# Optimization experiments

Measured on AMD Instinct MI355X. Metric: run time of the kernel, lower is better.

The kernel has to match this reference:

```python
import jax, jax.numpy as jnp
import numpy as np

L, H, HD, D, FF, V, S_LEN = 12, 12, 64, 768, 3072, 50257, 1024
NEG = jnp.finfo(jnp.float32).min


def _ln(x, g, b, eps=1e-5):
    mu = x.mean(-1, keepdims=True)
    var = ((x - mu) ** 2).mean(-1, keepdims=True)
    return (x - mu) * jax.lax.rsqrt(var + eps) * g + b


def setup_inputs() -> dict:
    key = jax.random.key(0)
    ks = jax.random.split(key, 14)
    n = lambda k, shp, s=0.02: jax.random.normal(k, shp, jnp.float32) * s
    return {
        "input_ids": jax.random.randint(ks[0], (1, S_LEN), 0, V, dtype=jnp.int32),
        "attention_mask": jnp.ones((1, S_LEN), jnp.int32),
        "wte": n(ks[1], (V, D)),
        "wpe": n(ks[2], (S_LEN, D)),
        "ln1_g": 1.0 + n(ks[3], (L, D), 0.01),
        "ln1_b": n(ks[4], (L, D), 0.01),
        "W_qkv": n(ks[5], (L, D, 3 * D)),
        "b_qkv": n(ks[6], (L, 3 * D)),
        "W_o": n(ks[7], (L, D, D)),
        "b_o": n(ks[8], (L, D)),
        "ln2_g": 1.0 + n(ks[9], (L, D), 0.01),
        "ln2_b": n(ks[10], (L, D), 0.01),
        "W_fc": n(ks[11], (L, D, FF)),
        "b_fc": n(ks[12], (L, FF)),
        "W_proj": n(ks[13], (L, FF, D)),
        "b_proj": jnp.zeros((L, D), jnp.float32),
        "S": 20, "Sa1": 21, "S2": 600,
    }


def reference(input_ids, attention_mask, wte, wpe, ln1_g, ln1_b, W_qkv, b_qkv,
              W_o, b_o, ln2_g, ln2_b, W_fc, b_fc, W_proj, b_proj, S, Sa1, S2):
    T = input_ids.shape[-1]
    h0 = wte[input_ids[0]] + wpe[:T]                      # [T, D]
    causal = jnp.tril(jnp.ones((T, T), bool))
    add_mask = (1.0 - attention_mask[0].astype(jnp.float32)) * NEG  # [T]
    scale = 1.0 / np.sqrt(HD).astype(np.float32)

    def step(h, p):
        (l1g, l1b, Wqkv, bqkv, Wo, bo, l2g, l2b, Wfc, bfc, Wp, bp) = p
        xl = _ln(h, l1g, l1b)                             # pre-block LN, [T, D]
        # ---- standard GPT-2 block forward (advances hidden state) ----
        qkv = xl @ Wqkv + bqkv
        q, k, v = jnp.split(qkv, 3, axis=-1)
        q = q.reshape(T, H, HD).transpose(1, 0, 2)        # [H, T, HD]
        k = k.reshape(T, H, HD).transpose(1, 0, 2)
        v = v.reshape(T, H, HD).transpose(1, 0, 2)
        sc = jnp.einsum('hqd,hkd->hqk', q, k) * scale
        sc = jnp.where(causal, sc, NEG) + add_mask
        ctx = jnp.einsum('hqk,hkd->hqd', jax.nn.softmax(sc, axis=-1), v)
        attn_out = ctx.transpose(1, 0, 2).reshape(T, D) @ Wo + bo
        h2 = h + attn_out
        h_new = h2 + (jax.nn.gelu(_ln(h2, l2g, l2b) @ Wfc + bfc,
                                  approximate=True) @ Wp + bp)
        # ---- manual QK circuit decomposition (pre-block hidden state) ----
        Wq, Wk, _ = jnp.split(Wqkv, 3, axis=1)            # [D, D] each
        bq, bk, _ = jnp.split(bqkv, 3, axis=0)            # [D] each
        Wmhq = Wq.reshape(D, H, HD).transpose(1, 0, 2)    # [H, D, HD]
        Wmhk = Wk.reshape(D, H, HD).transpose(1, 0, 2)
        bqh = bq.reshape(H, HD)                           # [H, HD]
        bkh = bk.reshape(H, HD)
        qc = jnp.einsum('td,hdk->htk', xl, Wmhq)          # x W_q per head
        kc = jnp.einsum('td,hdk->htk', xl, Wmhk)          # x W_k per head
        term1 = jnp.einsum('hqk,htk->hqt', qc, kc)                 # x Wq Wk^T x^T
        term2 = jnp.einsum('hk,htk->ht', bqh, kc)[:, None, :]      # bq Wk^T x^T
        term3 = jnp.einsum('hqk,hk->hq', qc, bkh)[:, :, None]      # x Wq bk^T
        term4 = jnp.einsum('hk,hk->h', bqh, bkh)[:, None, None]    # bq bk^T
        scores = (term1 + term2 + term3 + term4) * scale
        aw = jax.nn.softmax(jnp.where(causal, scores, NEG), axis=-1)  # [H, T, T]
        dup = aw[:, S2, S]
        ind = aw[:, S2, Sa1]
        prev = aw[:, -1, S2]
        return h_new, (dup, ind, prev, prev)

    params = (ln1_g, ln1_b, W_qkv, b_qkv, W_o, b_o,
              ln2_g, ln2_b, W_fc, b_fc, W_proj, b_proj)
    _, (dup, ind, prev, name) = jax.lax.scan(step, h0, params)
    return dup, ind, prev, name   # each [L, H] = [12, 12]
```

## Files before the change

### kernel.cpp

```cpp
#include <hip/hip_runtime.h>
#include <hip/hip_bf16.h>
#include <math.h>

namespace {

constexpr int T = 1024;
constexpr int D = 768;
constexpr int FF = 3072;
constexpr int H = 12;
constexpr int HD = 64;
constexpr int L = 12;
constexpr float SCALE = 0.125f;
constexpr float MNEG = -1.0e30f;

typedef __attribute__((ext_vector_type(8))) short short8;
typedef __attribute__((ext_vector_type(4))) float floatx4;

__device__ inline unsigned short f2bf(float f) {
    __hip_bfloat16 h = __float2bfloat16(f);
    return *reinterpret_cast<unsigned short*>(&h);
}
__device__ inline float bf2f(unsigned short u) {
    union { unsigned int i; float f; } c;
    c.i = (unsigned int)u << 16;
    return c.f;
}
__device__ inline void gld16(const void* g, void* l) {
    __builtin_amdgcn_global_load_lds(
        (const __attribute__((address_space(1))) void*)g,
        (__attribute__((address_space(3))) void*)l, 16, 0, 0);
}

__global__ void embed_kernel(const int* __restrict__ ids,
                             const float* __restrict__ wte,
                             const float* __restrict__ wpe,
                             float* __restrict__ h) {
    int i = blockIdx.x * blockDim.x + threadIdx.x;
    if (i >= T * D) return;
    int t = i / D, d = i % D;
    h[i] = wte[(long)ids[t] * D + d] + wpe[i];
}

__global__ __launch_bounds__(256)
void ln_kernel(const float* __restrict__ x, const float* __restrict__ g,
               const float* __restrict__ b, unsigned short* __restrict__ out) {
    int row = blockIdx.x, tid = threadIdx.x;
    const float* xr = x + (long)row * D;
    float v0 = xr[tid], v1 = xr[tid + 256], v2 = xr[tid + 512];
    __shared__ float red[4];
    __shared__ float share;
    float s = v0 + v1 + v2;
#pragma unroll
    for (int o = 32; o; o >>= 1) s += __shfl_down(s, o, 64);
    if ((tid & 63) == 0) red[tid >> 6] = s;
    __syncthreads();
    if (tid == 0) share = (red[0] + red[1] + red[2] + red[3]) * (1.0f / D);
    __syncthreads();
    float mu = share;
    float d0 = v0 - mu, d1 = v1 - mu, d2 = v2 - mu;
    float q = d0 * d0 + d1 * d1 + d2 * d2;
#pragma unroll
    for (int o = 32; o; o >>= 1) q += __shfl_down(q, o, 64);
    __syncthreads();
    if ((tid & 63) == 0) red[tid >> 6] = q;
    __syncthreads();
    if (tid == 0) share = rsqrtf((red[0] + red[1] + red[2] + red[3]) * (1.0f / D) + 1e-5f);
    __syncthreads();
    float rs = share;
    unsigned short* orow = out + (long)row * D;
    orow[tid]       = f2bf(d0 * rs * g[tid]       + b[tid]);
    orow[tid + 256] = f2bf(d1 * rs * g[tid + 256] + b[tid + 256]);
    orow[tid + 512] = f2bf(d2 * rs * g[tid + 512] + b[tid + 512]);
}

__global__ __launch_bounds__(256)
void wconvert_b(const float* __restrict__ W, unsigned short* __restrict__ WT,
                int K, int N) {
    const int zl = blockIdx.z;
    W  += (long)zl * K * N;
    WT += (long)zl * N * K;
    __shared__ float t[32][33];
    const int n0 = blockIdx.x * 32, k0 = blockIdx.y * 32;
    const int tx = threadIdx.x, ty = threadIdx.y;
#pragma unroll
    for (int i = 0; i < 4; i++)
        t[ty * 4 + i][tx] = W[(long)(k0 + ty * 4 + i) * N + n0 + tx];
    __syncthreads();
#pragma unroll
    for (int i = 0; i < 4; i++)
        WT[(long)(n0 + ty * 4 + i) * K + k0 + tx] = f2bf(t[tx][ty * 4 + i]);
}

#define GEMM_CORE(KLEN)                                                                 \
    floatx4 acc[2][4] = {};                                                             \
    gld16(ApA, &As[0][ablk][0][0]);                                                     \
    gld16(ApB, &As[0][ablk + 4][0][0]);                                                 \
    gld16(Bp,  &Bs[0][ablk][0][0]);                                                     \
    __syncthreads();                                                                    \
    const int nsteps = (KLEN) >> 5;                                                     \
    for (int s = 0; s < nsteps; s++) {                                                  \
        const int buf = s & 1;                                                          \
        const int nb = buf ^ 1;                                                         \
        if (s + 1 < nsteps) {                                                           \
            gld16(ApA + (s + 1) * 32, &As[nb][ablk][0][0]);                             \
            gld16(ApB + (s + 1) * 32, &As[nb][ablk + 4][0][0]);                         \
            gld16(Bp  + (s + 1) * 32, &Bs[nb][ablk][0][0]);                             \
        }                                                                               \
        short8 af[2], bfr[4];                                                           \
        _Pragma("unroll")                                                               \
        for (int mi = 0; mi < 2; mi++)                                                  \
            af[mi] = *(const short8*)&As[buf][w * 2 + mi][lane][0];                     \
        _Pragma("unroll")                                                               \
        for (int ni = 0; ni < 4; ni++)                                                  \
            bfr[ni] = *(const short8*)&Bs[buf][ni][lane][0];                            \
        _Pragma("unroll")                                                               \
        for (int mi = 0; mi < 2; mi++)                                                  \
            _Pragma("unroll")                                                           \
            for (int ni = 0; ni < 4; ni++)                                              \
                acc[mi][ni] = __builtin_amdgcn_mfma_f32_16x16x32_bf16(                  \
                    af[mi], bfr[ni], acc[mi][ni], 0, 0, 0);                             \
        __syncthreads();                                                                \
    }

#define GEMM_PRELUDE(KOFF)                                                              \
    const int tid = threadIdx.x;                                                        \
    const int w = tid >> 6, lane = tid & 63;                                            \
    const int ablk = tid >> 6;                                                          \
    const int sl = tid & 63;                                                            \
    const int row0 = blockIdx.y * 128, col0 = blockIdx.x * 64;                          \
    __shared__ unsigned short As[2][8][64][8];                                          \
    __shared__ unsigned short Bs[2][4][64][8];                                          \
    const unsigned short* ApA = A + (long)(row0 + ablk * 16 + (sl & 15)) * K + (KOFF) + (sl >> 4) * 8; \
    const unsigned short* ApB = ApA + 64L * K;                                          \
    const unsigned short* Bp  = BT + (long)(col0 + ablk * 16 + (sl & 15)) * K + (KOFF) + (sl >> 4) * 8;

__global__ __launch_bounds__(256)
void gemm_fused(const unsigned short* __restrict__ A, const unsigned short* __restrict__ BT,
                const float* __restrict__ bias, unsigned short* __restrict__ Cb,
                int N, int K, int flags) {
    GEMM_PRELUDE(0)
    GEMM_CORE(K)
#pragma unroll
    for (int mi = 0; mi < 2; mi++) {
        int rg = row0 + (w * 2 + mi) * 16 + (lane >> 4) * 4;
#pragma unroll
        for (int ni = 0; ni < 4; ni++) {
            int cg = col0 + ni * 16 + (lane & 15);
            float bv = (flags & 1) ? bias[cg] : 0.f;
            float bscale = ((flags & 16) && cg < D) ? SCALE : 1.0f;
#pragma unroll
            for (int r = 0; r < 4; r++) {
                float v = acc[mi][ni][r] + bv;
                if (flags & 4) {
                    float zz = 0.7978845608028654f * (v + 0.044715f * v * v * v);
                    v = v / (1.0f + __expf(-2.0f * zz));
                }
                Cb[(long)(rg + r) * N + cg] = f2bf(v * bscale);
            }
        }
    }
}

__global__ __launch_bounds__(256)
void gemm_bf16(const unsigned short* __restrict__ A, const unsigned short* __restrict__ BT,
               float* __restrict__ part, int N, int K, int splitK) {
    const int z = blockIdx.z;
    const int Kc = K / splitK;
    GEMM_PRELUDE(z * Kc)
    GEMM_CORE(Kc)
    float* dst = part + (long)z * T * N;
#pragma unroll
    for (int mi = 0; mi < 2; mi++) {
        int rg = row0 + (w * 2 + mi) * 16 + (lane >> 4) * 4;
#pragma unroll
        for (int ni = 0; ni < 4; ni++) {
            int cg = col0 + ni * 16 + (lane & 15);
#pragma unroll
            for (int r = 0; r < 4; r++)
                dst[(long)(rg + r) * N + cg] = acc[mi][ni][r];
        }
    }
}

__global__ __launch_bounds__(256)
void reduce_ln(const float* __restrict__ part, const float* __restrict__ bias,
               const float* __restrict__ resid,
               const float* __restrict__ g, const float* __restrict__ b,
               float* __restrict__ Cres, unsigned short* __restrict__ Cln,
               int splitK) {
    const int row = blockIdx.x, tid = threadIdx.x;
    const int c0 = tid, c1 = tid + 256, c2 = tid + 512;
    const long rb = (long)row * D;
    float v0 = bias[c0] + resid[rb + c0];
    float v1 = bias[c1] + resid[rb + c1];
    float v2 = bias[c2] + resid[rb + c2];
    for (int z = 0; z < splitK; z++) {
        const float* p = part + (long)z * T * D + rb;
        v0 += p[c0]; v1 += p[c1]; v2 += p[c2];
    }
    float* crow = Cres + rb;
    crow[c0] = v0; crow[c1] = v1; crow[c2] = v2;
    __shared__ float red[4];
    __shared__ float share;
    float s = v0 + v1 + v2;
#pragma unroll
    for (int o = 32; o; o >>= 1) s += __shfl_down(s, o, 64);
    if ((tid & 63) == 0) red[tid >> 6] = s;
    __syncthreads();
    if (tid == 0) share = (red[0] + red[1] + red[2] + red[3]) * (1.0f / D);
    __syncthreads();
    float mu = share;
    float d0 = v0 - mu, d1 = v1 - mu, d2 = v2 - mu;
    float q = d0 * d0 + d1 * d1 + d2 * d2;
#pragma unroll
    for (int o = 32; o; o >>= 1) q += __shfl_down(q, o, 64);
    __syncthreads();
    if ((tid & 63) == 0) red[tid >> 6] = q;
    __syncthreads();
    if (tid == 0) share = rsqrtf((red[0] + red[1] + red[2] + red[3]) * (1.0f / D) + 1e-5f);
    __syncthreads();
    float rs = share;
    unsigned short* orow = Cln + rb;
    orow[c0] = f2bf(d0 * rs * g[c0] + b[c0]);
    orow[c1] = f2bf(d1 * rs * g[c1] + b[c1]);
    orow[c2] = f2bf(d2 * rs * g[c2] + b[c2]);
}

__device__ void probe_body(const unsigned short* __restrict__ qkvb,
                           const int* __restrict__ Sp, const int* __restrict__ Sa1p,
                           const int* __restrict__ S2p,
                           float* __restrict__ out, int layer, int which, int h) {
    const int s = *Sp, sa1 = *Sa1p, s2 = *S2p;
    const int row = which ? (T - 1) : s2;
    const int tid = threadIdx.x;
    __shared__ float qrow[64];
    __shared__ float prob[T];
    __shared__ float red[4];
    __shared__ float bshare;
    if (tid < 64) qrow[tid] = bf2f(qkvb[(long)row * (3 * D) + h * HD + tid]);
    __syncthreads();
    float mloc = -INFINITY;
    for (int j = tid; j <= row; j += 256) {
        const unsigned short* krow = qkvb + (long)j * (3 * D) + D + h * HD;
        float acc = 0;
#pragma unroll
        for (int d = 0; d < 64; d += 8) {
            short8 kv = *(const short8*)(krow + d);
#pragma unroll
            for (int e = 0; e < 8; e++)
                acc += qrow[d + e] * bf2f((unsigned short)kv[e]);
        }
        prob[j] = acc;
        mloc = fmaxf(mloc, acc);
    }
#pragma unroll
    for (int o = 32; o; o >>= 1) mloc = fmaxf(mloc, __shfl_down(mloc, o, 64));
    if ((tid & 63) == 0) red[tid >> 6] = mloc;
    __syncthreads();
    if (tid == 0) bshare = fmaxf(fmaxf(red[0], red[1]), fmaxf(red[2], red[3]));
    __syncthreads();
    float m = bshare;
    float ssum = 0;
    for (int j = tid; j <= row; j += 256) {
        float e = expf(prob[j] - m);
        prob[j] = e;
        ssum += e;
    }
#pragma unroll
    for (int o = 32; o; o >>= 1) ssum += __shfl_down(ssum, o, 64);
    __syncthreads();
    if ((tid & 63) == 0) red[tid >> 6] = ssum;
    __syncthreads();
    if (tid == 0) bshare = red[0] + red[1] + red[2] + red[3];
    __syncthreads();
    float inv = 1.0f / bshare;
    if (tid == 0) {
        if (which == 0) {
            out[0 * (L * H) + layer * H + h] = prob[s] * inv;
            out[1 * (L * H) + layer * H + h] = prob[sa1] * inv;
        } else {
            out[2 * (L * H) + layer * H + h] = prob[s2] * inv;
            out[3 * (L * H) + layer * H + h] = prob[s2] * inv;
        }
    }
}

__global__ __launch_bounds__(256)
void probe_kernel(const unsigned short* __restrict__ qkvb,
                  const int* __restrict__ Sp, const int* __restrict__ Sa1p,
                  const int* __restrict__ S2p,
                  float* __restrict__ out, int layer) {
    probe_body(qkvb, Sp, Sa1p, S2p, out, layer, blockIdx.x, blockIdx.y);
}

__global__ __launch_bounds__(256)
void flash_probe(const unsigned short* __restrict__ qkvb, unsigned short* __restrict__ ctxb,
                 const int* __restrict__ Sp, const int* __restrict__ Sa1p,
                 const int* __restrict__ S2p, float* __restrict__ out, int layer) {
    const int h = blockIdx.y;
    if (blockIdx.x >= T / 32) {
        probe_body(qkvb, Sp, Sa1p, S2p, out, layer, blockIdx.x - T / 32, h);
        return;
    }
    const int q0 = blockIdx.x * 32;
    const int tid = threadIdx.x;
    const int w = tid >> 6;
    const int pair = w >> 1;
    const int sub = w & 1;
    const int l = tid & 63;
    const int lm = l & 15;
    const int g = l >> 4;

    __shared__ unsigned short Kl[64][72];
    __shared__ unsigned short Vt[64][80];
    __shared__ unsigned short Pl[4][16][72];

    const int qw = q0 + pair * 16;

    short8 qf[2];
    {
        const unsigned short* qp = qkvb + (long)(qw + lm) * (3 * D) + h * HD + g * 8;
        qf[0] = *(const short8*)(qp);
        qf[1] = *(const short8*)(qp + 32);
    }

    const int d8 = (tid & 7) * 8;
    const int kp = (tid >> 3) * 2;

    float m = MNEG, lsum = 0.f;
    floatx4 o[4] = {};
    const int nt = blockIdx.x / 2 + 1;

    for (int t = 0; t < nt; t++) {
        const int c0 = t * 64;
        __syncthreads();
        {
            const unsigned short* kr0 = qkvb + (long)(c0 + kp) * (3 * D) + D + h * HD + d8;
            const unsigned short* kr1 = kr0 + 3 * D;
            *(short8*)&Kl[kp][d8]     = *(const short8*)kr0;
            *(short8*)&Kl[kp + 1][d8] = *(const short8*)kr1;
            short8 va = *(const short8*)(kr0 + D);
            short8 vb = *(const short8*)(kr1 + D);
#pragma unroll
            for (int j = 0; j < 8; j++) {
                unsigned int pk = (unsigned)(unsigned short)va[j] |
                                  ((unsigned)(unsigned short)vb[j] << 16);
                *(unsigned int*)&Vt[d8 + j][kp] = pk;
            }
        }
        __syncthreads();

        floatx4 st[2] = {};
#pragma unroll
        for (int ks = 0; ks < 2; ks++)
#pragma unroll
            for (int m2 = 0; m2 < 2; m2++) {
                short8 af = *(const short8*)&Kl[(sub * 2 + m2) * 16 + lm][ks * 32 + g * 8];
                st[m2] = __builtin_amdgcn_mfma_f32_16x16x32_bf16(af, qf[ks], st[m2], 0, 0, 0);
            }

        const int qg = qw + lm;
        const int cb = c0 + sub * 32;
        if (cb + 31 > qw) {
#pragma unroll
            for (int m2 = 0; m2 < 2; m2++)
#pragma unroll
                for (int r = 0; r < 4; r++)
                    if (cb + m2 * 16 + g * 4 + r > qg) st[m2][r] = MNEG;
        }
        float tmax = fmaxf(fmaxf(fmaxf(st[0][0], st[0][1]), fmaxf(st[0][2], st[0][3])),
                           fmaxf(fmaxf(st[1][0], st[1][1]), fmaxf(st[1][2], st[1][3])));
        tmax = fmaxf(tmax, __shfl_xor(tmax, 16));
        tmax = fmaxf(tmax, __shfl_xor(tmax, 32));
        float mn = fmaxf(m, tmax);
        float alpha = __expf(m - mn);
        float psum = 0.f;
        unsigned short pb[8];
#pragma unroll
        for (int m2 = 0; m2 < 2; m2++)
#pragma unroll
            for (int r = 0; r < 4; r++) {
                float p = __expf(st[m2][r] - mn);
                psum += p;
                pb[m2 * 4 + r] = f2bf(p);
            }
        lsum = lsum * alpha + psum;
        m = mn;
#pragma unroll
        for (int m2 = 0; m2 < 2; m2++) {
            unsigned int p0 = (unsigned)pb[m2 * 4 + 0] | ((unsigned)pb[m2 * 4 + 1] << 16);
            unsigned int p1 = (unsigned)pb[m2 * 4 + 2] | ((unsigned)pb[m2 * 4 + 3] << 16);
            *(unsigned int*)&Pl[w][lm][(sub * 2 + m2) * 16 + g * 4]     = p0;
            *(unsigned int*)&Pl[w][lm][(sub * 2 + m2) * 16 + g * 4 + 2] = p1;
        }
        float ar0 = __shfl(alpha, g * 4 + 0), ar1 = __shfl(alpha, g * 4 + 1);
        float ar2 = __shfl(alpha, g * 4 + 2), ar3 = __shfl(alpha, g * 4 + 3);
#pragma unroll
        for (int fd = 0; fd < 4; fd++) {
            o[fd][0] *= ar0; o[fd][1] *= ar1; o[fd][2] *= ar2; o[fd][3] *= ar3;
        }
        {
            short8 pa = *(const short8*)&Pl[w][lm][sub * 32 + g * 8];
#pragma unroll
            for (int fd = 0; fd < 4; fd++) {
                short8 vb = *(const short8*)&Vt[fd * 16 + lm][sub * 32 + g * 8];
                o[fd] = __builtin_amdgcn_mfma_f32_16x16x32_bf16(pa, vb, o[fd], 0, 0, 0);
            }
        }
    }
    float l2 = lsum + __shfl_xor(lsum, 16);
    float l4 = l2 + __shfl_xor(l2, 32);

    float* Om = (float*)&Kl[0][0];
    float2* Mlb = (float2*)((char*)Om + 2 * 16 * 68 * 4);
    __syncthreads();
    if (sub == 1) {
        if (g == 0) Mlb[pair * 16 + lm] = make_float2(m, l4);
#pragma unroll
        for (int fd = 0; fd < 4; fd++)
#pragma unroll
            for (int r = 0; r < 4; r++)
                Om[(pair * 16 + g * 4 + r) * 68 + fd * 16 + lm] = o[fd][r];
    }
    __syncthreads();
    if (sub == 0) {
        float2 oth = Mlb[pair * 16 + lm];
        float M = fmaxf(m, oth.x);
        float e0 = __expf(m - M), e1 = __expf(oth.x - M);
        float inv = 1.0f / (l4 * e0 + oth.y * e1);
        float a0 = e0 * inv, a1 = e1 * inv;
#pragma unroll
        for (int fd = 0; fd < 4; fd++) {
            unsigned short* cp = ctxb + (long)(qw + g * 4) * D + h * HD + fd * 16 + lm;
#pragma unroll
            for (int r = 0; r < 4; r++) {
                float w0r = __shfl(a0, g * 4 + r);
                float w1r = __shfl(a1, g * 4 + r);
                float val = o[fd][r] * w0r +
                            Om[(pair * 16 + g * 4 + r) * 68 + fd * 16 + lm] * w1r;
                cp[(long)r * D] = f2bf(val);
            }
        }
    }
}

}

extern "C" void kernel_launch(void* const* d_in, const int* in_sizes, int n_in,
                              void* d_out, int out_size, void* d_ws, size_t ws_size,
                              hipStream_t stream) {
    const int*   ids    = (const int*)  d_in[0];
    const float* wte    = (const float*)d_in[2];
    const float* wpe    = (const float*)d_in[3];
    const float* ln1_g  = (const float*)d_in[4];
    const float* ln1_b  = (const float*)d_in[5];
    const float* W_qkv  = (const float*)d_in[6];
    const float* b_qkv  = (const float*)d_in[7];
    const float* W_o    = (const float*)d_in[8];
    const float* b_o    = (const float*)d_in[9];
    const float* ln2_g  = (const float*)d_in[10];
    const float* ln2_b  = (const float*)d_in[11];
    const float* W_fc   = (const float*)d_in[12];
    const float* b_fc   = (const float*)d_in[13];
    const float* W_proj = (const float*)d_in[14];
    const float* b_proj = (const float*)d_in[15];
    const int*   Sp     = (const int*)  d_in[16];
    const int*   Sa1p   = (const int*)  d_in[17];
    const int*   S2p    = (const int*)  d_in[18];
    float* out = (float*)d_out;

    float* ws   = (float*)d_ws;
    float* h    = ws;
    float* h2   = h   + (long)T * D;
    float* part = h2  + (long)T * D;
    unsigned short* xl   = (unsigned short*)(part + 4L * T * D);
    unsigned short* qkvb = xl   + (long)T * D;
    unsigned short* ctxb = qkvb + (long)T * 3 * D;
    unsigned short* fb   = ctxb + (long)T * D;
    unsigned short* wt_qkv  = fb      + (long)T * FF;
    unsigned short* wt_o    = wt_qkv  + (long)L * 3 * D * D;
    unsigned short* wt_fc   = wt_o    + (long)L * D * D;
    unsigned short* wt_proj = wt_fc   + (long)L * D * FF;

    embed_kernel<<<(T * D + 255) / 256, 256, 0, stream>>>(ids, wte, wpe, h);
    wconvert_b<<<dim3(3 * D / 32, D / 32, L), dim3(32, 8), 0, stream>>>(W_qkv, wt_qkv, D, 3 * D);
    wconvert_b<<<dim3(D / 32, D / 32, L), dim3(32, 8), 0, stream>>>(W_o, wt_o, D, D);
    wconvert_b<<<dim3(FF / 32, D / 32, L), dim3(32, 8), 0, stream>>>(W_fc, wt_fc, D, FF);
    wconvert_b<<<dim3(D / 32, FF / 32, L), dim3(32, 8), 0, stream>>>(W_proj, wt_proj, FF, D);
    ln_kernel<<<T, 256, 0, stream>>>(h, ln1_g, ln1_b, xl);

    for (int l = 0; l < L; l++) {
        gemm_fused<<<dim3(3 * D / 64, T / 128), 256, 0, stream>>>(
            xl, wt_qkv + (long)l * 3 * D * D, b_qkv + (long)l * 3 * D,
            qkvb, 3 * D, D, 1 | 16);

        if (l == L - 1) {
            probe_kernel<<<dim3(2, H), 256, 0, stream>>>(qkvb, Sp, Sa1p, S2p, out, l);
            break;
        }

        flash_probe<<<dim3(T / 32 + 2, H), 256, 0, stream>>>(
            qkvb, ctxb, Sp, Sa1p, S2p, out, l);
        gemm_bf16<<<dim3(D / 64, T / 128, 4), 256, 0, stream>>>(
            ctxb, wt_o + (long)l * D * D, part, D, D, 4);
        reduce_ln<<<T, 256, 0, stream>>>(
            part, b_o + (long)l * D, h, ln2_g + l * D, ln2_b + l * D, h2, xl, 4);
        gemm_fused<<<dim3(FF / 64, T / 128), 256, 0, stream>>>(
            xl, wt_fc + (long)l * D * FF, b_fc + (long)l * FF, fb, FF, D, 1 | 4);
        gemm_bf16<<<dim3(D / 64, T / 128, 4), 256, 0, stream>>>(
            fb, wt_proj + (long)l * D * FF, part, D, FF, 4);
        reduce_ln<<<T, 256, 0, stream>>>(
            part, b_proj + (long)l * D, h2, ln1_g + (l + 1) * D, ln1_b + (l + 1) * D, h, xl, 4);
    }
}
```

Before: 1.338 ms.

## Double GEMM K-step to 64 and load attention K fragments directly from global

The shared GEMM core now stages 64-wide K slices per pipeline step (two 32-wide sub-tiles), which halves the number of barrier/prefetch iterations and doubles the shared-memory tiles. The flash attention kernel stops staging K in LDS and has each wave read its K MFMA fragments straight from global memory, with dedicated LDS buffers added for the final merge. The aim is fewer syncs and less LDS traffic, at the cost of more LDS per GEMM block (possibly lower occupancy) and uncoalesced, L2-dependent K reads in attention.

```diff
diff --git a/kernel.cpp b/kernel.cpp
--- a/kernel.cpp
+++ b/kernel.cpp
@@ -93,32 +93,42 @@
 
 #define GEMM_CORE(KLEN)                                                                 \
     floatx4 acc[2][4] = {};                                                             \
-    gld16(ApA, &As[0][ablk][0][0]);                                                     \
-    gld16(ApB, &As[0][ablk + 4][0][0]);                                                 \
-    gld16(Bp,  &Bs[0][ablk][0][0]);                                                     \
+    gld16(ApA,      &As[0][ablk][0][0][0]);                                             \
+    gld16(ApA + 32, &As[0][ablk][1][0][0]);                                             \
+    gld16(ApB,      &As[0][ablk + 4][0][0][0]);                                         \
+    gld16(ApB + 32, &As[0][ablk + 4][1][0][0]);                                         \
+    gld16(Bp,       &Bs[0][ablk][0][0][0]);                                             \
+    gld16(Bp + 32,  &Bs[0][ablk][1][0][0]);                                             \
     __syncthreads();                                                                    \
-    const int nsteps = (KLEN) >> 5;                                                     \
+    const int nsteps = (KLEN) >> 6;                                                     \
     for (int s = 0; s < nsteps; s++) {                                                  \
         const int buf = s & 1;                                                          \
         const int nb = buf ^ 1;                                                         \
         if (s + 1 < nsteps) {                                                           \
-            gld16(ApA + (s + 1) * 32, &As[nb][ablk][0][0]);                             \
-            gld16(ApB + (s + 1) * 32, &As[nb][ablk + 4][0][0]);                         \
-            gld16(Bp  + (s + 1) * 32, &Bs[nb][ablk][0][0]);                             \
+            const long ko = (long)(s + 1) * 64;                                         \
+            gld16(ApA + ko,      &As[nb][ablk][0][0][0]);                               \
+            gld16(ApA + ko + 32, &As[nb][ablk][1][0][0]);                               \
+            gld16(ApB + ko,      &As[nb][ablk + 4][0][0][0]);                           \
+            gld16(ApB + ko + 32, &As[nb][ablk + 4][1][0][0]);                           \
+            gld16(Bp + ko,       &Bs[nb][ablk][0][0][0]);                               \
+            gld16(Bp + ko + 32,  &Bs[nb][ablk][1][0][0]);                               \
         }                                                                               \
-        short8 af[2], bfr[4];                                                           \
         _Pragma("unroll")                                                               \
-        for (int mi = 0; mi < 2; mi++)                                                  \
-            af[mi] = *(const short8*)&As[buf][w * 2 + mi][lane][0];                     \
-        _Pragma("unroll")                                                               \
-        for (int ni = 0; ni < 4; ni++)                                                  \
-            bfr[ni] = *(const short8*)&Bs[buf][ni][lane][0];                            \
-        _Pragma("unroll")                                                               \
-        for (int mi = 0; mi < 2; mi++)                                                  \
+        for (int ks = 0; ks < 2; ks++) {                                                \
+            short8 af[2], bfr[4];                                                       \
+            _Pragma("unroll")                                                           \
+            for (int mi = 0; mi < 2; mi++)                                              \
+                af[mi] = *(const short8*)&As[buf][w * 2 + mi][ks][lane][0];             \
             _Pragma("unroll")                                                           \
             for (int ni = 0; ni < 4; ni++)                                              \
-                acc[mi][ni] = __builtin_amdgcn_mfma_f32_16x16x32_bf16(                  \
-                    af[mi], bfr[ni], acc[mi][ni], 0, 0, 0);                             \
+                bfr[ni] = *(const short8*)&Bs[buf][ni][ks][lane][0];                    \
+            _Pragma("unroll")                                                           \
+            for (int mi = 0; mi < 2; mi++)                                              \
+                _Pragma("unroll")                                                       \
+                for (int ni = 0; ni < 4; ni++)                                          \
+                    acc[mi][ni] = __builtin_amdgcn_mfma_f32_16x16x32_bf16(              \
+                        af[mi], bfr[ni], acc[mi][ni], 0, 0, 0);                         \
+        }                                                                               \
         __syncthreads();                                                                \
     }
 
@@ -128,8 +138,8 @@
     const int ablk = tid >> 6;                                                          \
     const int sl = tid & 63;                                                            \
     const int row0 = blockIdx.y * 128, col0 = blockIdx.x * 64;                          \
-    __shared__ unsigned short As[2][8][64][8];                                          \
-    __shared__ unsigned short Bs[2][4][64][8];                                          \
+    __shared__ unsigned short As[2][8][2][64][8];                                       \
+    __shared__ unsigned short Bs[2][4][2][64][8];                                       \
     const unsigned short* ApA = A + (long)(row0 + ablk * 16 + (sl & 15)) * K + (KOFF) + (sl >> 4) * 8; \
     const unsigned short* ApB = ApA + 64L * K;                                          \
     const unsigned short* Bp  = BT + (long)(col0 + ablk * 16 + (sl & 15)) * K + (KOFF) + (sl >> 4) * 8;
@@ -311,9 +321,10 @@
     const int lm = l & 15;
     const int g = l >> 4;
 
-    __shared__ unsigned short Kl[64][72];
     __shared__ unsigned short Vt[64][80];
     __shared__ unsigned short Pl[4][16][72];
+    __shared__ float Om[2][16][68];
+    __shared__ float2 Mlb[2][16];
 
     const int qw = q0 + pair * 16;
 
@@ -323,6 +334,7 @@
         qf[0] = *(const short8*)(qp);
         qf[1] = *(const short8*)(qp + 32);
     }
+    const unsigned short* kfb = qkvb + (long)lm * (3 * D) + D + h * HD + g * 8;
 
     const int d8 = (tid & 7) * 8;
     const int kp = (tid >> 3) * 2;
@@ -335,12 +347,10 @@
         const int c0 = t * 64;
         __syncthreads();
         {
-            const unsigned short* kr0 = qkvb + (long)(c0 + kp) * (3 * D) + D + h * HD + d8;
-            const unsigned short* kr1 = kr0 + 3 * D;
-            *(short8*)&Kl[kp][d8]     = *(const short8*)kr0;
-            *(short8*)&Kl[kp + 1][d8] = *(const short8*)kr1;
-            short8 va = *(const short8*)(kr0 + D);
-            short8 vb = *(const short8*)(kr1 + D);
+            const unsigned short* vr0 = qkvb + (long)(c0 + kp) * (3 * D) + 2 * D + h * HD + d8;
+            const unsigned short* vr1 = vr0 + 3 * D;
+            short8 va = *(const short8*)vr0;
+            short8 vb = *(const short8*)vr1;
 #pragma unroll
             for (int j = 0; j < 8; j++) {
                 unsigned int pk = (unsigned)(unsigned short)va[j] |
@@ -355,7 +365,8 @@
         for (int ks = 0; ks < 2; ks++)
 #pragma unroll
             for (int m2 = 0; m2 < 2; m2++) {
-                short8 af = *(const short8*)&Kl[(sub * 2 + m2) * 16 + lm][ks * 32 + g * 8];
+                short8 af = *(const short8*)(kfb +
+                    (long)(c0 + (sub * 2 + m2) * 16) * (3 * D) + ks * 32);
                 st[m2] = __builtin_amdgcn_mfma_f32_16x16x32_bf16(af, qf[ks], st[m2], 0, 0, 0);
             }
 
@@ -411,20 +422,18 @@
     float l2 = lsum + __shfl_xor(lsum, 16);
     float l4 = l2 + __shfl_xor(l2, 32);
 
-    float* Om = (float*)&Kl[0][0];
-    float2* Mlb = (float2*)((char*)Om + 2 * 16 * 68 * 4);
     __syncthreads();
     if (sub == 1) {
-        if (g == 0) Mlb[pair * 16 + lm] = make_float2(m, l4);
+        if (g == 0) Mlb[pair][lm] = make_float2(m, l4);
 #pragma unroll
         for (int fd = 0; fd < 4; fd++)
 #pragma unroll
             for (int r = 0; r < 4; r++)
-                Om[(pair * 16 + g * 4 + r) * 68 + fd * 16 + lm] = o[fd][r];
+                Om[pair][g * 4 + r][fd * 16 + lm] = o[fd][r];
     }
     __syncthreads();
     if (sub == 0) {
-        float2 oth = Mlb[pair * 16 + lm];
+        float2 oth = Mlb[pair][lm];
         float M = fmaxf(m, oth.x);
         float e0 = __expf(m - M), e1 = __expf(oth.x - M);
         float inv = 1.0f / (l4 * e0 + oth.y * e1);
@@ -436,8 +445,7 @@
             for (int r = 0; r < 4; r++) {
                 float w0r = __shfl(a0, g * 4 + r);
                 float w1r = __shfl(a1, g * 4 + r);
-                float val = o[fd][r] * w0r +
-                            Om[(pair * 16 + g * 4 + r) * 68 + fd * 16 + lm] * w1r;
+                float val = o[fd][r] * w0r + Om[pair][g * 4 + r][fd * 16 + lm] * w1r;
                 cp[(long)r * D] = f2bf(val);
             }
         }
```

New measurement: 1.381 ms. 1.03x slower.
